# Optimization experiments

Measured on AMD Instinct MI355X. Metric: run time of the kernel, lower is better.

Reference implementation:

```python
import jax, jax.numpy as jnp
import numpy as np

EMBED = 1024
HEADS = 16
HEAD_DIM = EMBED // HEADS
LN_EPS = 1e-5


def setup_inputs() -> dict:
    key = jax.random.key(0)
    ks = jax.random.split(key, 7)
    B, S = 2, 2048
    x = jax.random.normal(ks[0], (B, S, EMBED), dtype=jnp.float32)
    attn_params = jax.random.uniform(ks[1], (B, S, 3 * EMBED), dtype=jnp.float32)
    sc = 1.0 / np.sqrt(EMBED)
    Wqkv = jax.random.normal(ks[2], (3 * EMBED, EMBED), dtype=jnp.float32) * sc
    Wout = jax.random.normal(ks[3], (EMBED, EMBED), dtype=jnp.float32) * sc
    b_out = jnp.zeros((EMBED,), dtype=jnp.float32)
    gamma = jnp.ones((EMBED,), dtype=jnp.float32)
    beta = jnp.zeros((EMBED,), dtype=jnp.float32)
    return {"x": x, "attn_params": attn_params, "Wqkv": Wqkv, "Wout": Wout,
            "b_out": b_out, "gamma": gamma, "beta": beta}


def reference(x, attn_params, Wqkv, Wout, b_out, gamma, beta):
    B, S, E = x.shape
    # qkv projection (no bias) followed by elementwise attn_params scaling
    qkv = jnp.einsum('bse,fe->bsf', x, Wqkv) * attn_params  # [B,S,3E]
    q, k, v = jnp.split(qkv, 3, axis=-1)
    # [B,H,S,D]
    q = q.reshape(B, S, HEADS, HEAD_DIM).transpose(0, 2, 1, 3)
    k = k.reshape(B, S, HEADS, HEAD_DIM).transpose(0, 2, 1, 3)
    v = v.reshape(B, S, HEADS, HEAD_DIM).transpose(0, 2, 1, 3)
    scores = jnp.einsum('bhqd,bhkd->bhqk', q, k) / jnp.sqrt(jnp.float32(HEAD_DIM))
    attn = jax.nn.softmax(scores, axis=-1)
    weighted = jnp.einsum('bhqk,bhkd->bhqd', attn, v)  # [B,H,S,D]
    weighted = weighted.transpose(0, 2, 1, 3).reshape(B, S, E)
    out = jnp.einsum('bse,fe->bsf', weighted, Wout) + b_out
    out = out + x  # residual
    # layernorm over last dim
    mu = jnp.mean(out, axis=-1, keepdims=True)
    var = jnp.mean(jnp.square(out - mu), axis=-1, keepdims=True)
    return (out - mu) * jax.lax.rsqrt(var + LN_EPS) * gamma + beta
```

## Files before the change

kernel.cpp:

```cpp
#include <hip/hip_runtime.h>

typedef float f32x4 __attribute__((ext_vector_type(4)));
typedef short s16x8 __attribute__((ext_vector_type(8)));
typedef unsigned short u16;

#define AS1 __attribute__((address_space(1)))
#define AS3 __attribute__((address_space(3)))

__device__ __forceinline__ u16 f2bf(float f){
    union { float f; unsigned u; } v; v.f = f;
    unsigned r = v.u + 0x7FFFu + ((v.u >> 16) & 1u);
    return (u16)(r >> 16);
}

__device__ __forceinline__ void pswap(unsigned &A, unsigned &B){
    asm("v_permlane32_swap_b32 %0, %1\n\tv_permlane16_swap_b32 %0, %1" : "+v"(A), "+v"(B));
}
__device__ __forceinline__ unsigned cvtpk(float lo, float hi){
    unsigned w;
    asm("v_cvt_pk_bf16_f32 %0, %1, %2" : "=v"(w) : "v"(lo), "v"(hi));
    return w;
}

__global__ __launch_bounds__(256) void cvt3_bf16(
    const float* __restrict__ a, u16* __restrict__ da, int na,
    const float* __restrict__ b, u16* __restrict__ db, int nb,
    const float* __restrict__ c, u16* __restrict__ dc, int nc)
{
    int i = blockIdx.x * 256 + threadIdx.x;
    const float* s; u16* d; int off;
    if (i < na){ s = a; d = da; off = i; }
    else if (i < na + nb){ s = b; d = db; off = i - na; }
    else if (i < na + nb + nc){ s = c; d = dc; off = i - na - nb; }
    else return;
    float4 v = ((const float4*)s)[off];
    ushort4 o;
    o.x = f2bf(v.x); o.y = f2bf(v.y); o.z = f2bf(v.z); o.w = f2bf(v.w);
    ((ushort4*)d)[off] = o;
}

__global__ __launch_bounds__(512, 2) void gemm256(
    const u16* __restrict__ A, const u16* __restrict__ Bw,
    int N, int K,
    const float* __restrict__ e0, u16* __restrict__ Cout)
{
    __shared__ u16 lds[2][4][128 * 64];
    const int tid = threadIdx.x;
    const int w = tid >> 6, l = tid & 63;
    const int g = l >> 4, c = l & 15;
    const int wm = w >> 2, wn = w & 3;
    const int sg = (g ^ (((c >> 3) & 1) << 1) ^ ((c >> 2) & 1)) << 4;

    const int bid = blockIdx.x;
    const int xcd = bid & 7, lin = bid >> 3;
    const int rowBase = (xcd * 2 + (lin & 1)) * 256;
    const int colBase = (lin >> 1) * 256;

    const int s_r_lo = l >> 2;
    const int s_col  = ((l & 3) ^ (((l >> 5) & 1) << 1) ^ ((l >> 4) & 1)) * 8;

    f32x4 acc[8][4] = {};

#define SBAR() asm volatile("s_barrier" ::: "memory")
#define VMW(n) asm volatile("s_waitcnt vmcnt(" #n ")" ::: "memory")

#define STAGE_A(bb, r, j_) do{                                                             \
    _Pragma("unroll")                                                                      \
    for (int i_ = 0; i_ < 2; ++i_){                                                        \
        int st_ = i_ * 8 + w;                                                              \
        int rg_ = st_ >> 1;                                                                \
        int row_ = (rg_ >> 2) * 128 + (r) * 64 + (rg_ & 3) * 16 + s_r_lo;                  \
        int col_ = (st_ & 1) * 32 + s_col;                                                 \
        const u16* src_ = A + (size_t)(rowBase + row_) * K + ((j_) * 64 + col_);           \
        __builtin_amdgcn_global_load_lds((const AS1 void*)src_,                            \
            (AS3 void*)((char*)&lds[bb][r][0] + st_ * 1024), 16, 0, 0);                    \
    } }while(0)

#define STAGE_B(bb, s, j_) do{                                                             \
    _Pragma("unroll")                                                                      \
    for (int i_ = 0; i_ < 2; ++i_){                                                        \
        int st_ = i_ * 8 + w;                                                              \
        int rg_ = st_ >> 1;                                                                \
        int row_ = (rg_ >> 1) * 64 + (s) * 32 + (rg_ & 1) * 16 + s_r_lo;                   \
        int col_ = (st_ & 1) * 32 + s_col;                                                 \
        const u16* src_ = Bw + (size_t)(colBase + row_) * K + ((j_) * 64 + col_);          \
        __builtin_amdgcn_global_load_lds((const AS1 void*)src_,                            \
            (AS3 void*)((char*)&lds[bb][2 + (s)][0] + st_ * 1024), 16, 0, 0);              \
    } }while(0)

#define LDA(bb, mh) do{                                                                    \
    _Pragma("unroll") for (int mi_ = 0; mi_ < 4; ++mi_){                                   \
        _Pragma("unroll") for (int kk_ = 0; kk_ < 2; ++kk_){                               \
            a2[mi_][kk_] = *(const s16x8*)((const char*)&lds[bb][mh][0] +                  \
                ((((wm * 4 + mi_) * 2 + kk_) << 10) + c * 64 + sg));                       \
        } } }while(0)

#define LDB(bb, nh) do{                                                                    \
    _Pragma("unroll") for (int ni_ = 0; ni_ < 2; ++ni_){                                   \
        _Pragma("unroll") for (int kk_ = 0; kk_ < 2; ++kk_){                               \
            bfr[nh][ni_][kk_] = *(const s16x8*)((const char*)&lds[bb][2 + (nh)][0] +       \
                ((((wn * 2 + ni_) * 2 + kk_) << 10) + c * 64 + sg));                       \
        } } }while(0)

#define MFMAQ(mh, nh) do{                                                                  \
    __builtin_amdgcn_s_setprio(1);                                                         \
    _Pragma("unroll") for (int mi_ = 0; mi_ < 4; ++mi_){                                   \
        _Pragma("unroll") for (int ni_ = 0; ni_ < 2; ++ni_){                               \
            _Pragma("unroll") for (int kk_ = 0; kk_ < 2; ++kk_){                           \
                acc[(mh)*4+mi_][(nh)*2+ni_] = __builtin_amdgcn_mfma_f32_16x16x32_bf16(     \
                    a2[mi_][kk_], bfr[nh][ni_][kk_], acc[(mh)*4+mi_][(nh)*2+ni_], 0,0,0);  \
            } } }                                                                          \
    __builtin_amdgcn_s_setprio(0);                                                         \
}while(0)

    const int ntk = K >> 6;

    STAGE_A(0, 0, 0); STAGE_B(0, 0, 0); STAGE_B(0, 1, 0); STAGE_A(0, 1, 0);
    STAGE_A(1, 0, 1); STAGE_B(1, 0, 1); STAGE_B(1, 1, 1); STAGE_A(1, 1, 1);
    VMW(8);
    SBAR();

    s16x8 a2[4][2];
    s16x8 bfr[2][2][2];
#pragma unroll 2
    for (int t = 0; t < ntk; ++t){
        const int cur = t & 1;
        const bool pf = (t + 2 < ntk);

        LDA(cur, 0);
        LDB(cur, 0);
        SBAR();
        MFMAQ(0, 0);
        SBAR();

        LDB(cur, 1);
        if (pf) STAGE_A(cur, 0, t + 2);
        SBAR();
        MFMAQ(0, 1);
        SBAR();

        LDA(cur, 1);
        if (pf) STAGE_B(cur, 0, t + 2);
        SBAR();
        MFMAQ(1, 0);
        SBAR();

        if (pf){ STAGE_A(cur, 1, t + 2); STAGE_B(cur, 1, t + 2); }
        SBAR();
        MFMAQ(1, 1);
        SBAR();

        if (t + 1 < ntk){
            if (pf) VMW(8); else VMW(0);
            SBAR();
        }
    }

#pragma unroll
    for (int mt = 0; mt < 8; ++mt){
        const int rbase = rowBase + wm * 128 + mt * 16 + g * 4;
        float ev[16];
#pragma unroll
        for (int nt_ = 0; nt_ < 4; ++nt_){
            const int cc = colBase + wn * 64 + nt_ * 16 + c;
#pragma unroll
            for (int jj = 0; jj < 4; ++jj)
                ev[nt_ * 4 + jj] = e0[(size_t)(rbase + jj) * N + cc];
        }
#pragma unroll
        for (int nt_ = 0; nt_ < 4; ++nt_){
            const int cc = colBase + wn * 64 + nt_ * 16 + c;
#pragma unroll
            for (int jj = 0; jj < 4; ++jj){
                float apv = ev[nt_ * 4 + jj];
                if (cc < 1024) apv *= 0.18033688f;
                Cout[(size_t)(rbase + jj) * N + cc] = f2bf(acc[mt][nt_][jj] * apv);
            }
        }
    }
#undef STAGE_A
#undef STAGE_B
#undef LDA
#undef LDB
#undef MFMAQ
#undef SBAR
#undef VMW
}

__global__ __launch_bounds__(256) void gemm_bt(
    const u16* __restrict__ A, const u16* __restrict__ Bw,
    int M, int N, int K,
    const float* __restrict__ e0, const float* __restrict__ e1,
    float* __restrict__ Cout)
{
    __shared__ u16 As[2][128 * 32];
    __shared__ u16 Bs[2][128 * 32];
    const int tid = threadIdx.x;
    const int w = tid >> 6, lane = tid & 63;
    const int g = lane >> 4, c = lane & 15;
    const int wr = w >> 1, wc = w & 1;
    const int rowBase = blockIdx.y * 128;
    const int colBase = blockIdx.x * 128;

    f32x4 acc[4][4] = {};

    auto STAGE = [&](int pb, int k0){
#pragma unroll
        for (int i = 0; i < 2; ++i){
            int o  = i * 4096 + tid * 16;
            int r  = o >> 6;
            int ce = (o & 63) >> 1;
            const u16* ga = A  + (size_t)(rowBase + r) * K + (k0 + ce);
            __builtin_amdgcn_global_load_lds((const AS1 void*)ga,
                (AS3 void*)((char*)As[pb] + i * 4096 + w * 1024), 16, 0, 0);
            const u16* gb = Bw + (size_t)(colBase + r) * K + (k0 + ce);
            __builtin_amdgcn_global_load_lds((const AS1 void*)gb,
                (AS3 void*)((char*)Bs[pb] + i * 4096 + w * 1024), 16, 0, 0);
        }
    };

    const int nt = K >> 5;
    STAGE(0, 0);
    __syncthreads();

    for (int t = 0; t < nt; ++t){
        const int cur = t & 1;
        if (t + 1 < nt) STAGE(cur ^ 1, (t + 1) * 32);

        s16x8 af[4], bfr[4];
#pragma unroll
        for (int m = 0; m < 4; ++m){
            int row = wr * 64 + m * 16 + c;
            af[m] = *(const s16x8*)((const char*)As[cur] + row * 64 + g * 16);
        }
#pragma unroll
        for (int n = 0; n < 4; ++n){
            int row = wc * 64 + n * 16 + c;
            bfr[n] = *(const s16x8*)((const char*)Bs[cur] + row * 64 + g * 16);
        }
#pragma unroll
        for (int m = 0; m < 4; ++m)
#pragma unroll
            for (int n = 0; n < 4; ++n)
                acc[m][n] = __builtin_amdgcn_mfma_f32_16x16x32_bf16(af[m], bfr[n], acc[m][n], 0, 0, 0);
        __syncthreads();
    }

    float bcol[4];
#pragma unroll
    for (int n = 0; n < 4; ++n)
        bcol[n] = e0[colBase + wc * 64 + n * 16 + c];

#pragma unroll
    for (int m = 0; m < 4; ++m){
        const int rbase = rowBase + wr * 64 + m * 16 + g * 4;
        float ev[16];
#pragma unroll
        for (int n = 0; n < 4; ++n){
            const int cc = colBase + wc * 64 + n * 16 + c;
#pragma unroll
            for (int j = 0; j < 4; ++j)
                ev[n * 4 + j] = e1[(size_t)(rbase + j) * N + cc];
        }
#pragma unroll
        for (int n = 0; n < 4; ++n){
            const int cc = colBase + wc * 64 + n * 16 + c;
#pragma unroll
            for (int j = 0; j < 4; ++j)
                Cout[(size_t)(rbase + j) * N + cc] = acc[m][n][j] + bcol[n] + ev[n * 4 + j];
        }
    }
}

__global__ __launch_bounds__(256) void vtrans(const u16* __restrict__ qkv, u16* __restrict__ vt){
    __shared__ u16 t_[64 * 64];
    int bh = blockIdx.x; int b = bh >> 4; int h = bh & 15;
    int st = blockIdx.y;
    int tid = threadIdx.x;
#pragma unroll
    for (int i = 0; i < 2; ++i){
        int id = i * 256 + tid;
        int sr = id >> 3, c8 = id & 7;
        uint4 v = *(const uint4*)(qkv + (size_t)(b * 2048 + st * 64 + sr) * 3072 + 2048 + h * 64 + c8 * 8);
        *(uint4*)((char*)t_ + ((sr * 128 + c8 * 16) ^ ((sr & 7) << 4))) = v;
    }
    __syncthreads();
#pragma unroll
    for (int i = 0; i < 2; ++i){
        int id = i * 256 + tid;
        int d = id >> 3, s8 = (id & 7) * 8;
        u16 tmp[8];
#pragma unroll
        for (int jj = 0; jj < 8; ++jj){
            int s = s8 + jj;
            tmp[jj] = *(const u16*)((const char*)t_ + ((s * 128 + d * 2) ^ ((s & 7) << 4)));
        }
        *(uint4*)(vt + ((size_t)bh * 64 + d) * 2048 + st * 64 + s8) = *(uint4*)tmp;
    }
}

__global__ __launch_bounds__(512) void attn_k(const u16* __restrict__ qkv,
                                              const u16* __restrict__ vt,
                                              u16* __restrict__ o)
{
    __shared__ u16 Kl[2][64 * 64];
    __shared__ u16 Vl[2][64 * 64];
    int bh = blockIdx.x; int b = bh >> 4, h = bh & 15;
    int qt = blockIdx.y;
    int tid = threadIdx.x;
    int w = tid >> 6, lane = tid & 63, g = lane >> 4, c = lane & 15;

    const size_t qrow = (size_t)(b * 2048 + qt * 128 + w * 16 + c);
    s16x8 qf[2];
    qf[0] = *(const s16x8*)(qkv + qrow * 3072 + h * 64 + g * 8);
    qf[1] = *(const s16x8*)(qkv + qrow * 3072 + h * 64 + 32 + g * 8);

    const s16x8 ones8 = {16256, 16256, 16256, 16256, 16256, 16256, 16256, 16256};

    f32x4 oa[4] = {};
    f32x4 la = {};

    int kr = tid >> 3, c8 = tid & 7;
    const u16* kg = qkv + (size_t)(b * 2048 + kr) * 3072 + 1024 + h * 64 + c8 * 8;
    const u16* vg = vt + ((size_t)bh * 64 + kr) * 2048 + c8 * 8;
    const int so = (kr * 128 + c8 * 16) ^ ((kr & 7) << 4);

    uint4 ks = *(const uint4*)kg;
    uint4 vs = *(const uint4*)vg;
    *(uint4*)((char*)Kl[0] + so) = ks;
    *(uint4*)((char*)Vl[0] + so) = vs;
    __syncthreads();

    for (int t = 0; t < 32; ++t){
        const int cur = t & 1;
        if (t < 31){
            ks = *(const uint4*)(kg + (size_t)(t + 1) * 64 * 3072);
            vs = *(const uint4*)(vg + (t + 1) * 64);
        }

        f32x4 st[4];
        __builtin_amdgcn_s_setprio(1);
#pragma unroll
        for (int kt = 0; kt < 4; ++kt){
            int row = kt * 16 + c;
            s16x8 kf0 = *(const s16x8*)((const char*)Kl[cur] + ((row * 128 + g * 16) ^ ((row & 7) << 4)));
            s16x8 kf1 = *(const s16x8*)((const char*)Kl[cur] + ((row * 128 + 64 + g * 16) ^ ((row & 7) << 4)));
            f32x4 a = {};
            a = __builtin_amdgcn_mfma_f32_16x16x32_bf16(kf0, qf[0], a, 0, 0, 0);
            a = __builtin_amdgcn_mfma_f32_16x16x32_bf16(kf1, qf[1], a, 0, 0, 0);
            st[kt] = a;
        }
        __builtin_amdgcn_s_setprio(0);

        unsigned W[4][2];
#pragma unroll
        for (int kt = 0; kt < 4; ++kt){
            float p0 = __builtin_amdgcn_exp2f(st[kt][0]);
            float p1 = __builtin_amdgcn_exp2f(st[kt][1]);
            float p2 = __builtin_amdgcn_exp2f(st[kt][2]);
            float p3 = __builtin_amdgcn_exp2f(st[kt][3]);
            W[kt][0] = cvtpk(p0, p1);
            W[kt][1] = cvtpk(p2, p3);
        }

        __builtin_amdgcn_s_setprio(1);
#pragma unroll
        for (int kb = 0; kb < 2; ++kb){
            unsigned t0 = W[kb * 2][0], t2 = W[kb * 2 + 1][0];
            pswap(t0, t2);
            unsigned t1 = W[kb * 2][1], t3 = W[kb * 2 + 1][1];
            pswap(t1, t3);
            union { unsigned u[4]; s16x8 v; } pu;
            pu.u[0] = t0; pu.u[1] = t1; pu.u[2] = t2; pu.u[3] = t3;
#pragma unroll
            for (int dt = 0; dt < 4; ++dt){
                int vrow = dt * 16 + c;
                s16x8 vf = *(const s16x8*)((const char*)Vl[cur] + ((vrow * 128 + kb * 64 + g * 16) ^ ((vrow & 7) << 4)));
                oa[dt] = __builtin_amdgcn_mfma_f32_16x16x32_bf16(vf, pu.v, oa[dt], 0, 0, 0);
            }
            la = __builtin_amdgcn_mfma_f32_16x16x32_bf16(ones8, pu.v, la, 0, 0, 0);
        }
        __builtin_amdgcn_s_setprio(0);

        if (t < 31){
            *(uint4*)((char*)Kl[cur ^ 1] + so) = ks;
            *(uint4*)((char*)Vl[cur ^ 1] + so) = vs;
        }
        __syncthreads();
    }

    float inv = 1.0f / la[0];
#pragma unroll
    for (int dt = 0; dt < 4; ++dt){
        u16 t4[4];
#pragma unroll
        for (int j = 0; j < 4; ++j) t4[j] = f2bf(oa[dt][j] * inv);
        *(uint2*)(o + qrow * 1024 + h * 64 + dt * 16 + g * 4) = *(uint2*)t4;
    }
}

__global__ __launch_bounds__(256) void ln_k(const float* __restrict__ tmp,
                                            const float* __restrict__ gamma,
                                            const float* __restrict__ beta,
                                            float* __restrict__ out)
{
    int row = blockIdx.x;
    int tid = threadIdx.x;
    float4 v = ((const float4*)(tmp + (size_t)row * 1024))[tid];
    float s  = v.x + v.y + v.z + v.w;
    float ss = v.x * v.x + v.y * v.y + v.z * v.z + v.w * v.w;
    for (int m = 1; m < 64; m <<= 1){ s += __shfl_xor(s, m); ss += __shfl_xor(ss, m); }
    __shared__ float red[8];
    int w = tid >> 6;
    if ((tid & 63) == 0){ red[w * 2] = s; red[w * 2 + 1] = ss; }
    __syncthreads();
    s  = red[0] + red[2] + red[4] + red[6];
    ss = red[1] + red[3] + red[5] + red[7];
    float mu  = s * (1.f / 1024.f);
    float var = ss * (1.f / 1024.f) - mu * mu;
    float inv = rsqrtf(var + 1e-5f);
    float4 g4 = ((const float4*)gamma)[tid];
    float4 b4 = ((const float4*)beta)[tid];
    float4 r;
    r.x = (v.x - mu) * inv * g4.x + b4.x;
    r.y = (v.y - mu) * inv * g4.y + b4.y;
    r.z = (v.z - mu) * inv * g4.z + b4.z;
    r.w = (v.w - mu) * inv * g4.w + b4.w;
    ((float4*)(out + (size_t)row * 1024))[tid] = r;
}

extern "C" void kernel_launch(void* const* d_in, const int* in_sizes, int n_in,
                              void* d_out, int out_size, void* d_ws, size_t ws_size,
                              hipStream_t stream)
{
    const float* x     = (const float*)d_in[0];
    const float* ap    = (const float*)d_in[1];
    const float* wqkv  = (const float*)d_in[2];
    const float* wout  = (const float*)d_in[3];
    const float* bout  = (const float*)d_in[4];
    const float* gamma = (const float*)d_in[5];
    const float* beta  = (const float*)d_in[6];
    float* out = (float*)d_out;

    char* ws = (char*)d_ws;
    u16* xb    = (u16*)ws;  ws += (size_t)4096 * 1024 * 2;
    u16* wqkvb = (u16*)ws;  ws += (size_t)3072 * 1024 * 2;
    u16* woutb = (u16*)ws;  ws += (size_t)1024 * 1024 * 2;
    u16* qkvb  = (u16*)ws;  ws += (size_t)4096 * 3072 * 2;
    u16* vtb   = (u16*)ws;  ws += (size_t)32 * 64 * 2048 * 2;
    u16* attnb = (u16*)ws;  ws += (size_t)4096 * 1024 * 2;
    float* tmp = (float*)ws;

    const int na = 4096 * 1024 / 4, nb = 3072 * 1024 / 4, nc = 1024 * 1024 / 4;
    cvt3_bf16<<<(na + nb + nc + 255) / 256, 256, 0, stream>>>(x, xb, na, wqkv, wqkvb, nb, wout, woutb, nc);

    gemm256<<<192, 512, 0, stream>>>(xb, wqkvb, 3072, 1024, ap, qkvb);
    vtrans<<<dim3(32, 32), 256, 0, stream>>>(qkvb, vtb);
    attn_k<<<dim3(32, 16), 512, 0, stream>>>(qkvb, vtb, attnb);
    gemm_bt<<<dim3(8, 32), 256, 0, stream>>>(attnb, woutb, 4096, 1024, 1024, bout, x, tmp);
    ln_k<<<4096, 256, 0, stream>>>(tmp, gamma, beta, out);
}
```

Baseline: 136.2 us.

## Reschedule QKV GEMM main loop to overlap A-half staging and drop a barrier

```diff
diff --git a/kernel.cpp b/kernel.cpp
--- a/kernel.cpp
+++ b/kernel.cpp
@@ -62,7 +62,6 @@
     f32x4 acc[8][4] = {};
 
 #define SBAR() asm volatile("s_barrier" ::: "memory")
-#define VMW(n) asm volatile("s_waitcnt vmcnt(" #n ")" ::: "memory")
 
 #define STAGE_A(bb, r, j_) do{                                                             \
     _Pragma("unroll")                                                                      \
@@ -95,20 +94,20 @@
                 ((((wm * 4 + mi_) * 2 + kk_) << 10) + c * 64 + sg));                       \
         } } }while(0)
 
-#define LDB(bb, nh) do{                                                                    \
+#define LDB(bb, nh, dst) do{                                                               \
     _Pragma("unroll") for (int ni_ = 0; ni_ < 2; ++ni_){                                   \
         _Pragma("unroll") for (int kk_ = 0; kk_ < 2; ++kk_){                               \
-            bfr[nh][ni_][kk_] = *(const s16x8*)((const char*)&lds[bb][2 + (nh)][0] +       \
+            dst[ni_][kk_] = *(const s16x8*)((const char*)&lds[bb][2 + (nh)][0] +           \
                 ((((wn * 2 + ni_) * 2 + kk_) << 10) + c * 64 + sg));                       \
         } } }while(0)
 
-#define MFMAQ(mh, nh) do{                                                                  \
+#define MFMAQ(mh, nh, B) do{                                                               \
     __builtin_amdgcn_s_setprio(1);                                                         \
     _Pragma("unroll") for (int mi_ = 0; mi_ < 4; ++mi_){                                   \
         _Pragma("unroll") for (int ni_ = 0; ni_ < 2; ++ni_){                               \
             _Pragma("unroll") for (int kk_ = 0; kk_ < 2; ++kk_){                           \
                 acc[(mh)*4+mi_][(nh)*2+ni_] = __builtin_amdgcn_mfma_f32_16x16x32_bf16(     \
-                    a2[mi_][kk_], bfr[nh][ni_][kk_], acc[(mh)*4+mi_][(nh)*2+ni_], 0,0,0);  \
+                    a2[mi_][kk_], B[ni_][kk_], acc[(mh)*4+mi_][(nh)*2+ni_], 0,0,0);        \
             } } }                                                                          \
     __builtin_amdgcn_s_setprio(0);                                                         \
 }while(0)
@@ -117,43 +116,42 @@
 
     STAGE_A(0, 0, 0); STAGE_B(0, 0, 0); STAGE_B(0, 1, 0); STAGE_A(0, 1, 0);
     STAGE_A(1, 0, 1); STAGE_B(1, 0, 1); STAGE_B(1, 1, 1); STAGE_A(1, 1, 1);
-    VMW(8);
+    asm volatile("s_waitcnt vmcnt(8)" ::: "memory");
     SBAR();
 
     s16x8 a2[4][2];
-    s16x8 bfr[2][2][2];
-#pragma unroll 2
+    s16x8 b0f[2][2], b1f[2][2];
     for (int t = 0; t < ntk; ++t){
-        const int cur = t & 1;
-        const bool pf = (t + 2 < ntk);
+        const int cur = t & 1, nxt = cur ^ 1;
 
         LDA(cur, 0);
-        LDB(cur, 0);
-        SBAR();
-        MFMAQ(0, 0);
-        SBAR();
-
-        LDB(cur, 1);
-        if (pf) STAGE_A(cur, 0, t + 2);
-        SBAR();
-        MFMAQ(0, 1);
+        LDB(cur, 0, b0f);
+        if (t >= 1 && t + 1 < ntk) STAGE_A(nxt, 1, t + 1);
+        SBAR();
+        MFMAQ(0, 0, b0f);
+        SBAR();
+
+        LDB(cur, 1, b1f);
+        if (t + 2 < ntk) STAGE_A(cur, 0, t + 2);
+        SBAR();
+        MFMAQ(0, 1, b1f);
         SBAR();
 
         LDA(cur, 1);
-        if (pf) STAGE_B(cur, 0, t + 2);
-        SBAR();
-        MFMAQ(1, 0);
-        SBAR();
-
-        if (pf){ STAGE_A(cur, 1, t + 2); STAGE_B(cur, 1, t + 2); }
-        SBAR();
-        MFMAQ(1, 1);
-        SBAR();
-
-        if (t + 1 < ntk){
-            if (pf) VMW(8); else VMW(0);
-            SBAR();
-        }
+        if (t + 2 < ntk) STAGE_B(cur, 0, t + 2);
+        SBAR();
+        MFMAQ(1, 1, b1f);
+        SBAR();
+
+        if (t + 2 < ntk){
+            STAGE_B(cur, 1, t + 2);
+            asm volatile("s_waitcnt vmcnt(6)" ::: "memory");
+        } else if (t + 1 < ntk){
+            asm volatile("s_waitcnt vmcnt(0)" ::: "memory");
+        }
+        SBAR();
+        MFMAQ(1, 0, b0f);
+        SBAR();
     }
 
 #pragma unroll
@@ -184,7 +182,6 @@
 #undef LDB
 #undef MFMAQ
 #undef SBAR
-#undef VMW
 }
 
 __global__ __launch_bounds__(256) void gemm_bt(
```

After: 134.3 us. No clear change (-1.4%).
